# Performance work log

Measured on AMD Instinct MI355X. Metric: run time of the kernel, lower is better.

Reference implementation:

```python
import jax, jax.numpy as jnp
import numpy as np

IN_F = 128
OUT_F = 128
SCALE = float(np.sqrt(OUT_F))

def swish(x):
    return x * jax.nn.sigmoid(x)

def setup_inputs() -> dict:
    key = jax.random.key(0)
    ks = jax.random.split(key, 10)
    B, A = 4, 4096
    s = 1.0 / np.sqrt(IN_F)
    return {
        "x": jax.random.normal(ks[0], (B, A, IN_F), dtype=jnp.float32),
        "connectivity": jax.random.normal(ks[1], (B, A, A), dtype=jnp.float32),
        "Wq": jax.random.uniform(ks[2], (IN_F, OUT_F), jnp.float32, -s, s),
        "Wk": jax.random.uniform(ks[3], (IN_F, OUT_F), jnp.float32, -s, s),
        "Wv": jax.random.uniform(ks[4], (IN_F, OUT_F), jnp.float32, -s, s),
        "W1": jax.random.uniform(ks[5], (OUT_F, OUT_F), jnp.float32, -s, s),
        "b1": jnp.zeros((OUT_F,), jnp.float32),
        "W2": jax.random.uniform(ks[6], (OUT_F, OUT_F), jnp.float32, -s, s),
        "b2": jnp.zeros((OUT_F,), jnp.float32),
        "gamma": jnp.ones((OUT_F,), jnp.float32),
        "beta": jnp.zeros((OUT_F,), jnp.float32),
    }

def reference(x, connectivity, Wq, Wk, Wv, W1, b1, W2, b2, gamma, beta):
    # Q,K,V projections (no bias): [B,A,D]
    Q = jnp.einsum('bah,hd->bad', x, Wq)
    K = jnp.einsum('bah,hd->bad', x, Wk)
    V = jnp.einsum('bah,hd->bad', x, Wv)
    # dense all-pairs scores with additive connectivity bias: [B,A,A]
    scores = jnp.einsum('bqd,bkd->bqk', Q, K) / SCALE + connectivity
    alpha = jax.nn.softmax(scores, axis=-1)
    # dropout p=0.0 / eval mode -> identity
    H = jnp.einsum('bqk,bkd->bqd', alpha, V)
    # Swish-MLP tail
    h = swish(H)
    h = h @ W1 + b1
    h = swish(h)
    h = h @ W2 + b2
    # LayerNorm over last dim (eps=1e-5 as torch default)
    mu = jnp.mean(h, axis=-1, keepdims=True)
    var = jnp.var(h, axis=-1, keepdims=True)
    return (h - mu) * jax.lax.rsqrt(var + 1e-5) * gamma + beta
```

## Files before the change

kernel.cpp:

```cpp
#include <hip/hip_runtime.h>

#define L2E 1.44269504088896340736f
#define INV_SCALE 0.08838834764831845f

typedef _Float16 half8 __attribute__((ext_vector_type(8)));
typedef float f32x4 __attribute__((ext_vector_type(4)));

__device__ __forceinline__ float exp2_fast(float x) {
#if __has_builtin(__builtin_amdgcn_exp2f)
  return __builtin_amdgcn_exp2f(x);
#else
  return exp2f(x);
#endif
}

__device__ __forceinline__ f32x4 mfma16(half8 a, half8 b, f32x4 c) {
  return __builtin_amdgcn_mfma_f32_16x16x32_f16(a, b, c, 0, 0, 0);
}

__device__ __forceinline__ void gload16(const void* g, void* l) {
  __builtin_amdgcn_global_load_lds(
      (const __attribute__((address_space(1))) void*)g,
      (__attribute__((address_space(3))) void*)l, 16, 0, 0);
}

__device__ __forceinline__ float swish_f(float v) {
  return v / (1.f + exp2_fast(-L2E * v));
}

template <int CTRL>
__device__ __forceinline__ float dppmov(float x) {
  int xi = __builtin_bit_cast(int, x);
  int r = __builtin_amdgcn_update_dpp(xi, xi, CTRL, 0xf, 0xf, false);
  return __builtin_bit_cast(float, r);
}
__device__ __forceinline__ float red16_max(float x) {
  x = fmaxf(x, dppmov<0xB1>(x));
  x = fmaxf(x, dppmov<0x4E>(x));
  x = fmaxf(x, dppmov<0x141>(x));
  x = fmaxf(x, dppmov<0x140>(x));
  return x;
}
__device__ __forceinline__ float red16_sum(float x) {
  x += dppmov<0xB1>(x);
  x += dppmov<0x4E>(x);
  x += dppmov<0x141>(x);
  x += dppmov<0x140>(x);
  return x;
}

__global__ __launch_bounds__(256) void prep_kernel(
    const float* __restrict__ Wq, const float* __restrict__ Wk,
    const float* __restrict__ Wv, const float* __restrict__ W1,
    const float* __restrict__ W2, _Float16* __restrict__ Wf) {
  const int g = blockIdx.x * 256 + threadIdx.x;
  const int mat = g >> 11, rem = g & 2047;
  const int f = rem >> 6, lane = rem & 63;
  const int n = (f >> 2) * 16 + (lane & 15);
  const int k0 = (f & 3) * 32 + (lane >> 4) * 8;
  const float* W = (mat == 0) ? Wq : (mat == 1) ? Wk : (mat == 2) ? Wv
                   : (mat == 3) ? W1 : W2;
  half8 h;
#pragma unroll
  for (int j = 0; j < 8; ++j) h[j] = (_Float16)W[(k0 + j) * 128 + n];
  *(half8*)(Wf + (size_t)g * 8) = h;
}

__global__ __launch_bounds__(256) void kv_kernel(
    const float* __restrict__ x, const _Float16* __restrict__ Wf,
    _Float16* __restrict__ Kg, _Float16* __restrict__ Vg) {
  __shared__ __align__(16) _Float16 sc[64 * 136];
  const int tid = threadIdx.x;
  const int w = tid >> 6, lane = tid & 63;
  const int n16 = lane & 15, quad = lane >> 4;
  const int blk = blockIdx.x;

  half8 xf[4];
  {
    const float* xr = x + (size_t)(blk * 64 + w * 16 + n16) * 128 + quad * 8;
#pragma unroll
    for (int kc = 0; kc < 4; ++kc) {
      float4 a = *(const float4*)(xr + kc * 32);
      float4 b = *(const float4*)(xr + kc * 32 + 4);
      half8 h;
      h[0] = (_Float16)a.x; h[1] = (_Float16)a.y;
      h[2] = (_Float16)a.z; h[3] = (_Float16)a.w;
      h[4] = (_Float16)b.x; h[5] = (_Float16)b.y;
      h[6] = (_Float16)b.z; h[7] = (_Float16)b.w;
      xf[kc] = h;
    }
  }

  for (int mat = 0; mat < 2; ++mat) {
    f32x4 acc[8];
#pragma unroll
    for (int ct = 0; ct < 8; ++ct) acc[ct] = f32x4{0.f, 0.f, 0.f, 0.f};
#pragma unroll
    for (int ct = 0; ct < 8; ++ct)
#pragma unroll
      for (int kc = 0; kc < 4; ++kc) {
        half8 wf = *(const half8*)(Wf +
            ((size_t)((mat + 1) * 32 + ct * 4 + kc) * 64 + lane) * 8);
        acc[ct] = mfma16(xf[kc], wf, acc[ct]);
      }
#pragma unroll
    for (int ct = 0; ct < 8; ++ct)
#pragma unroll
      for (int r = 0; r < 4; ++r)
        sc[(w * 16 + quad * 4 + r) * 136 + ct * 16 + n16] = (_Float16)acc[ct][r];
    __syncthreads();

    if (mat == 0) {
#pragma unroll
      for (int i = 0; i < 4; ++i) {
        const int c = tid + 256 * i;
        const int ln = c & 63, kc = (c >> 6) & 3, ct = (c >> 8) & 1, tl = (c >> 9) & 1;
        half8 v = *(const half8*)&sc[(tl * 32 + ct * 16 + (ln & 15)) * 136 +
                                     kc * 32 + (ln >> 4) * 8];
        *(half8*)(Kg + ((((size_t)(blk * 2 + tl)) * 2 + ct) * 4 + kc) * 512 + ln * 8) = v;
      }
    } else {
#pragma unroll
      for (int i = 0; i < 4; ++i) {
        const int c = tid + 256 * i;
        const int ln = c & 63, dt = (c >> 6) & 7, tl = (c >> 9) & 1;
        const int q2 = ln >> 4, nn = ln & 15;
        half8 v;
#pragma unroll
        for (int j = 0; j < 8; ++j)
          v[j] = sc[(tl * 32 + q2 * 8 + j) * 136 + dt * 16 + nn];
        *(half8*)(Vg + (((size_t)(blk * 2 + tl)) * 8 + dt) * 512 + ln * 8) = v;
      }
    }
    __syncthreads();
  }
}

__global__ __launch_bounds__(128) void flash_kernel(
    const float* __restrict__ x, const float* __restrict__ conn,
    const _Float16* __restrict__ Wf,
    const _Float16* __restrict__ Kg, const _Float16* __restrict__ Vg,
    _Float16* __restrict__ Og, float2* __restrict__ Ml,
    int nsplit, int nt) {
  __shared__ __align__(16) _Float16 kb[2][4096];
  __shared__ __align__(16) _Float16 vb[2][4096];
  __shared__ __align__(16) _Float16 pb[2][656];

  const int tid = threadIdx.x, w = tid >> 6, lane = tid & 63;
  const int n16 = lane & 15, quad = lane >> 4;
  const int bid = blockIdx.x;
  const int sk = bid & (nsplit - 1);
  const int rest = (nsplit == 2) ? (bid >> 1) : bid;
  const int batch = rest & 3;
  const int rg = rest >> 2;
  const int rt_g = batch * 256 + rg * 2 + w;
  const int t0 = sk * nt;

  half8 qf[4];
  {
    half8 xf[4];
    const float* xr = x + (size_t)(batch * 4096 + rg * 32 + w * 16 + n16) * 128 + quad * 8;
#pragma unroll
    for (int kc = 0; kc < 4; ++kc) {
      float4 a = *(const float4*)(xr + kc * 32);
      float4 b = *(const float4*)(xr + kc * 32 + 4);
      half8 h;
      h[0] = (_Float16)a.x; h[1] = (_Float16)a.y;
      h[2] = (_Float16)a.z; h[3] = (_Float16)a.w;
      h[4] = (_Float16)b.x; h[5] = (_Float16)b.y;
      h[6] = (_Float16)b.z; h[7] = (_Float16)b.w;
      xf[kc] = h;
    }
    _Float16* tw = &kb[w][0];
#pragma unroll
    for (int ct = 0; ct < 8; ++ct) {
      f32x4 aq = f32x4{0.f, 0.f, 0.f, 0.f};
#pragma unroll
      for (int kc = 0; kc < 4; ++kc) {
        half8 wf = *(const half8*)(Wf + ((size_t)(ct * 4 + kc) * 64 + lane) * 8);
        aq = mfma16(xf[kc], wf, aq);
      }
#pragma unroll
      for (int r = 0; r < 4; ++r)
        tw[(quad * 4 + r) * 136 + ct * 16 + n16] = (_Float16)aq[r];
    }
#pragma unroll
    for (int kc = 0; kc < 4; ++kc)
      qf[kc] = *(const half8*)(tw + n16 * 136 + kc * 32 + quad * 8);
  }
  __syncthreads();

  const _Float16* Kt = Kg + (size_t)batch * 524288;
  const _Float16* Vt = Vg + (size_t)batch * 524288;
  const float* cp = conn + (size_t)batch * 16777216 +
                    (size_t)(rg * 32 + w * 16 + quad * 4) * 4096 + n16 +
                    (size_t)t0 * 32;
  const int wbase = (tid & ~63) * 8;

  auto stage = [&](int t, int buf) {
    const _Float16* ks = Kt + (size_t)t * 4096 + tid * 8;
    const _Float16* vs = Vt + (size_t)t * 4096 + tid * 8;
#pragma unroll
    for (int c = 0; c < 4; ++c) {
      gload16(ks + c * 1024, &kb[buf][c * 1024 + wbase]);
      gload16(vs + c * 1024, &vb[buf][c * 1024 + wbase]);
    }
  };
  float cc[8], cn[8];
  auto ldconn = [&](int i, float* cr) {
    const float* c0 = cp + (size_t)i * 32;
#pragma unroll
    for (int ct = 0; ct < 2; ++ct)
#pragma unroll
      for (int r = 0; r < 4; ++r)
        cr[ct * 4 + r] = c0[(size_t)r * 4096 + ct * 16] * L2E;
  };

  f32x4 o[8];
#pragma unroll
  for (int dt = 0; dt < 8; ++dt) o[dt] = f32x4{0.f, 0.f, 0.f, 0.f};
  float m_i[4] = {-__builtin_inff(), -__builtin_inff(),
                  -__builtin_inff(), -__builtin_inff()};
  float l_i[4] = {0.f, 0.f, 0.f, 0.f};

  stage(t0, 0);
  ldconn(0, cc);
  __syncthreads();

#pragma unroll 1
  for (int i = 0; i < nt; ++i) {
    const int cur = i & 1, nxt = cur ^ 1;
    if (i + 1 < nt) {
      stage(t0 + i + 1, nxt);
      ldconn(i + 1, cn);
    }
    f32x4 s0 = f32x4{0.f, 0.f, 0.f, 0.f};
    f32x4 s1 = f32x4{0.f, 0.f, 0.f, 0.f};
#pragma unroll
    for (int kc = 0; kc < 4; ++kc) {
      half8 kf0 = *(const half8*)&kb[cur][(0 * 4 + kc) * 512 + lane * 8];
      half8 kf1 = *(const half8*)&kb[cur][(1 * 4 + kc) * 512 + lane * 8];
      s0 = mfma16(qf[kc], kf0, s0);
      s1 = mfma16(qf[kc], kf1, s1);
    }
    const float c1 = L2E * INV_SCALE;
    float pr[8];
#pragma unroll
    for (int r = 0; r < 4; ++r) pr[r] = fmaf(s0[r], c1, cc[r]);
#pragma unroll
    for (int r = 0; r < 4; ++r) pr[4 + r] = fmaf(s1[r], c1, cc[4 + r]);
    float mt[4];
#pragma unroll
    for (int r = 0; r < 4; ++r) mt[r] = red16_max(fmaxf(pr[r], pr[4 + r]));
    int upd = (mt[0] > m_i[0]) | (mt[1] > m_i[1]) |
              (mt[2] > m_i[2]) | (mt[3] > m_i[3]);
    if (__any(upd)) {
#pragma unroll
      for (int r = 0; r < 4; ++r) {
        const float mn = fmaxf(m_i[r], mt[r]);
        const float al = exp2_fast(m_i[r] - mn);
        m_i[r] = mn;
        l_i[r] *= al;
#pragma unroll
        for (int dt = 0; dt < 8; ++dt) o[dt][r] *= al;
      }
    }
#pragma unroll
    for (int c = 0; c < 8; ++c) pr[c] = exp2_fast(pr[c] - m_i[c & 3]);
#pragma unroll
    for (int r = 0; r < 4; ++r) l_i[r] += red16_sum(pr[r] + pr[4 + r]);
    _Float16* pw = pb[w];
#pragma unroll
    for (int c = 0; c < 8; ++c)
      pw[(quad * 4 + (c & 3)) * 40 + (c >> 2) * 16 + n16] = (_Float16)pr[c];
    half8 pf = *(const half8*)(pw + n16 * 40 + quad * 8);
#pragma unroll
    for (int dt = 0; dt < 8; ++dt) {
      half8 vf = *(const half8*)&vb[cur][dt * 512 + lane * 8];
      o[dt] = mfma16(pf, vf, o[dt]);
    }
#pragma unroll
    for (int c = 0; c < 8; ++c) cc[c] = cn[c];
    __syncthreads();
  }

  float il[4];
#pragma unroll
  for (int r = 0; r < 4; ++r) il[r] = 1.f / l_i[r];
  _Float16* tw = &kb[w][0];
#pragma unroll
  for (int dt = 0; dt < 8; ++dt)
#pragma unroll
    for (int r = 0; r < 4; ++r)
      tw[(quad * 4 + r) * 136 + dt * 16 + n16] = (_Float16)(o[dt][r] * il[r]);
  _Float16* ob = Og + ((size_t)(sk * 1024 + rt_g) * 4) * 512;
#pragma unroll
  for (int kc = 0; kc < 4; ++kc) {
    half8 of = *(const half8*)(tw + n16 * 136 + kc * 32 + quad * 8);
    *(half8*)(ob + kc * 512 + lane * 8) = of;
  }
  if (n16 == 0) {
#pragma unroll
    for (int r = 0; r < 4; ++r)
      Ml[sk * 16384 + rt_g * 16 + quad * 4 + r] = make_float2(m_i[r], l_i[r]);
  }
}

__global__ __launch_bounds__(256) void mlp_kernel(
    const _Float16* __restrict__ Og, const float2* __restrict__ Ml,
    const _Float16* __restrict__ Wf,
    const float* __restrict__ b1, const float* __restrict__ b2,
    const float* __restrict__ gamma, const float* __restrict__ beta,
    float* __restrict__ out, int nsplit) {
  __shared__ __align__(16) _Float16 hb[4][2176];
  const int tid = threadIdx.x, w = tid >> 6, lane = tid & 63;
  const int n16 = lane & 15, quad = lane >> 4;
  const int rt_g = blockIdx.x * 4 + w;

  float2 ml[2];
  float m = -__builtin_inff();
  for (int s = 0; s < nsplit; ++s) {
    ml[s] = Ml[s * 16384 + rt_g * 16 + n16];
    m = fmaxf(m, ml[s].x);
  }
  float wgt[2], wsum = 0.f;
  for (int s = 0; s < nsplit; ++s) {
    wgt[s] = ml[s].y * exp2_fast(ml[s].x - m);
    wsum += wgt[s];
  }
  const float inv = 1.f / wsum;

  half8 hf[4];
#pragma unroll
  for (int kc = 0; kc < 4; ++kc) {
    float hv[8] = {0, 0, 0, 0, 0, 0, 0, 0};
    for (int s = 0; s < nsplit; ++s) {
      half8 ofr = *(const half8*)(Og +
          ((size_t)(s * 1024 + rt_g) * 4 + kc) * 512 + lane * 8);
#pragma unroll
      for (int j = 0; j < 8; ++j) hv[j] += wgt[s] * (float)ofr[j];
    }
    half8 h;
#pragma unroll
    for (int j = 0; j < 8; ++j) h[j] = (_Float16)swish_f(hv[j] * inv);
    hf[kc] = h;
  }

  float b1v[8], b2v[8], gv[8], bv[8];
#pragma unroll
  for (int ct = 0; ct < 8; ++ct) {
    b1v[ct] = b1[ct * 16 + n16];
    b2v[ct] = b2[ct * 16 + n16];
    gv[ct] = gamma[ct * 16 + n16];
    bv[ct] = beta[ct * 16 + n16];
  }

  f32x4 acc[8];
#pragma unroll
  for (int ct = 0; ct < 8; ++ct) acc[ct] = f32x4{0.f, 0.f, 0.f, 0.f};
#pragma unroll
  for (int ct = 0; ct < 8; ++ct)
#pragma unroll
    for (int kc = 0; kc < 4; ++kc) {
      half8 wf = *(const half8*)(Wf +
          ((size_t)(3 * 32 + ct * 4 + kc) * 64 + lane) * 8);
      acc[ct] = mfma16(hf[kc], wf, acc[ct]);
    }
  _Float16* hw = hb[w];
#pragma unroll
  for (int ct = 0; ct < 8; ++ct)
#pragma unroll
    for (int r = 0; r < 4; ++r)
      hw[(quad * 4 + r) * 136 + ct * 16 + n16] =
          (_Float16)swish_f(acc[ct][r] + b1v[ct]);
  half8 h1f[4];
#pragma unroll
  for (int kc = 0; kc < 4; ++kc)
    h1f[kc] = *(const half8*)(hw + n16 * 136 + kc * 32 + quad * 8);

#pragma unroll
  for (int ct = 0; ct < 8; ++ct) acc[ct] = f32x4{0.f, 0.f, 0.f, 0.f};
#pragma unroll
  for (int ct = 0; ct < 8; ++ct)
#pragma unroll
    for (int kc = 0; kc < 4; ++kc) {
      half8 wf = *(const half8*)(Wf +
          ((size_t)(4 * 32 + ct * 4 + kc) * 64 + lane) * 8);
      acc[ct] = mfma16(h1f[kc], wf, acc[ct]);
    }
  float hx[8][4];
  float sm[4] = {0, 0, 0, 0}, ss[4] = {0, 0, 0, 0};
#pragma unroll
  for (int ct = 0; ct < 8; ++ct)
#pragma unroll
    for (int r = 0; r < 4; ++r) {
      const float v = acc[ct][r] + b2v[ct];
      hx[ct][r] = v;
      sm[r] += v;
      ss[r] += v * v;
    }
#pragma unroll
  for (int r = 0; r < 4; ++r) {
    sm[r] = red16_sum(sm[r]);
    ss[r] = red16_sum(ss[r]);
  }
#pragma unroll
  for (int r = 0; r < 4; ++r) {
    const float mu = sm[r] * (1.f / 128.f);
    const float var = ss[r] * (1.f / 128.f) - mu * mu;
    const float rstd = rsqrtf(var + 1e-5f);
    const size_t row = (size_t)rt_g * 16 + quad * 4 + r;
#pragma unroll
    for (int ct = 0; ct < 8; ++ct)
      out[row * 128 + ct * 16 + n16] = (hx[ct][r] - mu) * rstd * gv[ct] + bv[ct];
  }
}

extern "C" void kernel_launch(void* const* d_in, const int* in_sizes, int n_in,
                              void* d_out, int out_size, void* d_ws,
                              size_t ws_size, hipStream_t stream) {
  const float* x     = (const float*)d_in[0];
  const float* conn  = (const float*)d_in[1];
  const float* Wq    = (const float*)d_in[2];
  const float* Wk    = (const float*)d_in[3];
  const float* Wv    = (const float*)d_in[4];
  const float* W1    = (const float*)d_in[5];
  const float* b1    = (const float*)d_in[6];
  const float* W2    = (const float*)d_in[7];
  const float* b2    = (const float*)d_in[8];
  const float* gamma = (const float*)d_in[9];
  const float* beta  = (const float*)d_in[10];
  float* out = (float*)d_out;

  const size_t need2 =
      ((size_t)81920 + 4 * 2097152) * 2 + 2 * 16384 * sizeof(float2);
  const int nsplit = (ws_size >= need2) ? 2 : 1;
  const int nt = 128 / nsplit;

  _Float16* Wf = (_Float16*)d_ws;
  _Float16* Kg = Wf + 81920;
  _Float16* Vg = Kg + 2097152;
  _Float16* Og = Vg + 2097152;
  float2* Ml = (float2*)(Og + (size_t)2097152 * nsplit);

  prep_kernel<<<40, 256, 0, stream>>>(Wq, Wk, Wv, W1, W2, Wf);
  kv_kernel<<<256, 256, 0, stream>>>(x, Wf, Kg, Vg);
  flash_kernel<<<512 * nsplit, 128, 0, stream>>>(x, conn, Wf, Kg, Vg, Og, Ml,
                                                 nsplit, nt);
  mlp_kernel<<<256, 256, 0, stream>>>(Og, Ml, Wf, b1, b2, gamma, beta, out,
                                      nsplit);
}
```

Before: 470.1 us.

## Transpose score MFMA so each lane owns one query row; vectorize connectivity loads

Swaps the MFMA operands for QK^T so that each lane holds scores for a single query row across 8 keys. Row max and sum then take two cross-lane shuffles instead of four DPP steps per row for four rows, and the connectivity bias becomes two float4 loads instead of eight strided scalar loads. The rescale factor for the output accumulator is passed through a small LDS buffer, the loop is unrolled by two with fixed buffer indices, and the block-to-batch mapping is reordered. Risks: extra LDS traffic and sync for the alpha broadcast, and a loop structure that assumes nt is even.

```diff
diff --git a/kernel.cpp b/kernel.cpp
--- a/kernel.cpp
+++ b/kernel.cpp
@@ -4,6 +4,7 @@
 #define INV_SCALE 0.08838834764831845f
 
 typedef _Float16 half8 __attribute__((ext_vector_type(8)));
+typedef _Float16 half4 __attribute__((ext_vector_type(4)));
 typedef float f32x4 __attribute__((ext_vector_type(4)));
 
 __device__ __forceinline__ float exp2_fast(float x) {
@@ -33,13 +34,6 @@
   int xi = __builtin_bit_cast(int, x);
   int r = __builtin_amdgcn_update_dpp(xi, xi, CTRL, 0xf, 0xf, false);
   return __builtin_bit_cast(float, r);
-}
-__device__ __forceinline__ float red16_max(float x) {
-  x = fmaxf(x, dppmov<0xB1>(x));
-  x = fmaxf(x, dppmov<0x4E>(x));
-  x = fmaxf(x, dppmov<0x141>(x));
-  x = fmaxf(x, dppmov<0x140>(x));
-  return x;
 }
 __device__ __forceinline__ float red16_sum(float x) {
   x += dppmov<0xB1>(x);
@@ -145,14 +139,17 @@
   __shared__ __align__(16) _Float16 kb[2][4096];
   __shared__ __align__(16) _Float16 vb[2][4096];
   __shared__ __align__(16) _Float16 pb[2][656];
+  __shared__ __align__(16) float alb[2][16];
 
   const int tid = threadIdx.x, w = tid >> 6, lane = tid & 63;
   const int n16 = lane & 15, quad = lane >> 4;
   const int bid = blockIdx.x;
-  const int sk = bid & (nsplit - 1);
-  const int rest = (nsplit == 2) ? (bid >> 1) : bid;
-  const int batch = rest & 3;
-  const int rg = rest >> 2;
+  int batch, sk, rg;
+  if (nsplit == 2) {
+    batch = bid & 3; sk = (bid >> 2) & 1; rg = bid >> 3;
+  } else {
+    batch = bid & 3; sk = 0; rg = bid >> 2;
+  }
   const int rt_g = batch * 256 + rg * 2 + w;
   const int t0 = sk * nt;
 
@@ -190,103 +187,119 @@
   }
   __syncthreads();
 
-  const _Float16* Kt = Kg + (size_t)batch * 524288;
-  const _Float16* Vt = Vg + (size_t)batch * 524288;
+  const _Float16* kp = Kg + (size_t)batch * 524288 + (size_t)t0 * 4096 + tid * 8;
+  const _Float16* vp = Vg + (size_t)batch * 524288 + (size_t)t0 * 4096 + tid * 8;
   const float* cp = conn + (size_t)batch * 16777216 +
-                    (size_t)(rg * 32 + w * 16 + quad * 4) * 4096 + n16 +
-                    (size_t)t0 * 32;
+                    (size_t)(rg * 32 + w * 16 + n16) * 4096 +
+                    (size_t)t0 * 32 + quad * 4;
   const int wbase = (tid & ~63) * 8;
 
   auto stage = [&](int t, int buf) {
-    const _Float16* ks = Kt + (size_t)t * 4096 + tid * 8;
-    const _Float16* vs = Vt + (size_t)t * 4096 + tid * 8;
+    const _Float16* ks = kp + (size_t)t * 4096;
+    const _Float16* vs = vp + (size_t)t * 4096;
 #pragma unroll
     for (int c = 0; c < 4; ++c) {
       gload16(ks + c * 1024, &kb[buf][c * 1024 + wbase]);
       gload16(vs + c * 1024, &vb[buf][c * 1024 + wbase]);
     }
   };
-  float cc[8], cn[8];
-  auto ldconn = [&](int i, float* cr) {
+  auto ldconn = [&](int i, float4* cr) {
     const float* c0 = cp + (size_t)i * 32;
-#pragma unroll
-    for (int ct = 0; ct < 2; ++ct)
-#pragma unroll
-      for (int r = 0; r < 4; ++r)
-        cr[ct * 4 + r] = c0[(size_t)r * 4096 + ct * 16] * L2E;
+    cr[0] = *(const float4*)c0;
+    cr[1] = *(const float4*)(c0 + 16);
   };
 
   f32x4 o[8];
 #pragma unroll
   for (int dt = 0; dt < 8; ++dt) o[dt] = f32x4{0.f, 0.f, 0.f, 0.f};
-  float m_i[4] = {-__builtin_inff(), -__builtin_inff(),
-                  -__builtin_inff(), -__builtin_inff()};
-  float l_i[4] = {0.f, 0.f, 0.f, 0.f};
-
-  stage(t0, 0);
-  ldconn(0, cc);
+  float m_i = -__builtin_inff();
+  float l_i = 0.f;
+
+  float4 ca[2], cb[2];
+  stage(0, 0);
+  ldconn(0, ca);
   __syncthreads();
 
-#pragma unroll 1
-  for (int i = 0; i < nt; ++i) {
-    const int cur = i & 1, nxt = cur ^ 1;
-    if (i + 1 < nt) {
-      stage(t0 + i + 1, nxt);
-      ldconn(i + 1, cn);
-    }
+  auto compute = [&](int buf, const float4* cc) {
     f32x4 s0 = f32x4{0.f, 0.f, 0.f, 0.f};
     f32x4 s1 = f32x4{0.f, 0.f, 0.f, 0.f};
+    const _Float16* kc_ = kb[buf];
 #pragma unroll
     for (int kc = 0; kc < 4; ++kc) {
-      half8 kf0 = *(const half8*)&kb[cur][(0 * 4 + kc) * 512 + lane * 8];
-      half8 kf1 = *(const half8*)&kb[cur][(1 * 4 + kc) * 512 + lane * 8];
-      s0 = mfma16(qf[kc], kf0, s0);
-      s1 = mfma16(qf[kc], kf1, s1);
-    }
-    const float c1 = L2E * INV_SCALE;
+      half8 kf0 = *(const half8*)&kc_[kc * 512 + lane * 8];
+      half8 kf1 = *(const half8*)&kc_[(4 + kc) * 512 + lane * 8];
+      s0 = mfma16(kf0, qf[kc], s0);
+      s1 = mfma16(kf1, qf[kc], s1);
+    }
     float pr[8];
 #pragma unroll
-    for (int r = 0; r < 4; ++r) pr[r] = fmaf(s0[r], c1, cc[r]);
-#pragma unroll
-    for (int r = 0; r < 4; ++r) pr[4 + r] = fmaf(s1[r], c1, cc[4 + r]);
-    float mt[4];
-#pragma unroll
-    for (int r = 0; r < 4; ++r) mt[r] = red16_max(fmaxf(pr[r], pr[4 + r]));
-    int upd = (mt[0] > m_i[0]) | (mt[1] > m_i[1]) |
-              (mt[2] > m_i[2]) | (mt[3] > m_i[3]);
-    if (__any(upd)) {
-#pragma unroll
-      for (int r = 0; r < 4; ++r) {
-        const float mn = fmaxf(m_i[r], mt[r]);
-        const float al = exp2_fast(m_i[r] - mn);
-        m_i[r] = mn;
-        l_i[r] *= al;
-#pragma unroll
-        for (int dt = 0; dt < 8; ++dt) o[dt][r] *= al;
-      }
-    }
-#pragma unroll
-    for (int c = 0; c < 8; ++c) pr[c] = exp2_fast(pr[c] - m_i[c & 3]);
-#pragma unroll
-    for (int r = 0; r < 4; ++r) l_i[r] += red16_sum(pr[r] + pr[4 + r]);
+    for (int r = 0; r < 4; ++r) {
+      pr[r] = fmaf(s0[r], INV_SCALE, cc[0][r]);
+      pr[4 + r] = fmaf(s1[r], INV_SCALE, cc[1][r]);
+    }
+    float mx = pr[0];
+#pragma unroll
+    for (int c = 1; c < 8; ++c) mx = fmaxf(mx, pr[c]);
+    mx = fmaxf(mx, __shfl_xor(mx, 16, 64));
+    mx = fmaxf(mx, __shfl_xor(mx, 32, 64));
+    if (__any(mx > m_i)) {
+      const float mn = fmaxf(m_i, mx);
+      const float al = exp2_fast((m_i - mn) * L2E);
+      m_i = mn;
+      l_i *= al;
+      if (quad == 0) alb[w][n16] = al;
+      const float4 av = *(const float4*)&alb[w][quad * 4];
+#pragma unroll
+      for (int dt = 0; dt < 8; ++dt)
+#pragma unroll
+        for (int r = 0; r < 4; ++r) o[dt][r] *= av[r];
+    }
+    const float nm = -m_i * L2E;
+#pragma unroll
+    for (int c = 0; c < 8; ++c) pr[c] = exp2_fast(fmaf(pr[c], L2E, nm));
+    float sm = pr[0];
+#pragma unroll
+    for (int c = 1; c < 8; ++c) sm += pr[c];
+    sm += __shfl_xor(sm, 16, 64);
+    sm += __shfl_xor(sm, 32, 64);
+    l_i += sm;
     _Float16* pw = pb[w];
-#pragma unroll
-    for (int c = 0; c < 8; ++c)
-      pw[(quad * 4 + (c & 3)) * 40 + (c >> 2) * 16 + n16] = (_Float16)pr[c];
+    half4 p0, p1;
+#pragma unroll
+    for (int r = 0; r < 4; ++r) {
+      p0[r] = (_Float16)pr[r];
+      p1[r] = (_Float16)pr[4 + r];
+    }
+    *(half4*)(pw + n16 * 40 + quad * 4) = p0;
+    *(half4*)(pw + n16 * 40 + 16 + quad * 4) = p1;
     half8 pf = *(const half8*)(pw + n16 * 40 + quad * 8);
+    const _Float16* vc = vb[buf];
 #pragma unroll
     for (int dt = 0; dt < 8; ++dt) {
-      half8 vf = *(const half8*)&vb[cur][dt * 512 + lane * 8];
+      half8 vf = *(const half8*)&vc[dt * 512 + lane * 8];
       o[dt] = mfma16(pf, vf, o[dt]);
     }
-#pragma unroll
-    for (int c = 0; c < 8; ++c) cc[c] = cn[c];
+  };
+
+#pragma unroll 1
+  for (int i = 0; i < nt; i += 2) {
+    stage(i + 1, 1);
+    ldconn(i + 1, cb);
+    compute(0, ca);
     __syncthreads();
-  }
-
+    if (i + 2 < nt) {
+      stage(i + 2, 0);
+      ldconn(i + 2, ca);
+    }
+    compute(1, cb);
+    __syncthreads();
+  }
+
+  if (quad == 0) alb[w][n16] = l_i;
+  const float4 lv = *(const float4*)&alb[w][quad * 4];
   float il[4];
 #pragma unroll
-  for (int r = 0; r < 4; ++r) il[r] = 1.f / l_i[r];
+  for (int r = 0; r < 4; ++r) il[r] = 1.f / lv[r];
   _Float16* tw = &kb[w][0];
 #pragma unroll
   for (int dt = 0; dt < 8; ++dt)
@@ -299,11 +312,8 @@
     half8 of = *(const half8*)(tw + n16 * 136 + kc * 32 + quad * 8);
     *(half8*)(ob + kc * 512 + lane * 8) = of;
   }
-  if (n16 == 0) {
-#pragma unroll
-    for (int r = 0; r < 4; ++r)
-      Ml[sk * 16384 + rt_g * 16 + quad * 4 + r] = make_float2(m_i[r], l_i[r]);
-  }
+  if (quad == 0)
+    Ml[sk * 16384 + rt_g * 16 + n16] = make_float2(m_i, l_i);
 }
 
 __global__ __launch_bounds__(256) void mlp_kernel(
@@ -325,7 +335,7 @@
   }
   float wgt[2], wsum = 0.f;
   for (int s = 0; s < nsplit; ++s) {
-    wgt[s] = ml[s].y * exp2_fast(ml[s].x - m);
+    wgt[s] = ml[s].y * exp2_fast((ml[s].x - m) * L2E);
     wsum += wgt[s];
   }
   const float inv = 1.f / wsum;
```

Measured after the change: 454.5 us. 3.3% less time.
